# Kernel tuning notes

Measured on AMD Instinct MI355X. Metric: run time of the kernel, lower is better.

Reference implementation:

```python
import jax, jax.numpy as jnp
import numpy as np

N_NODES = 50000
N_EDGES = 800000
D_IN = 256
D_HID = 256
N_CLASSES = 40


def gcn_conv(x, W, b, src, dst, deg_inv_sqrt, n):
    # PyG GCNConv: linear transform first, then normalized scatter-add aggregation.
    x = x @ W                                   # [N, d_out]
    norm = deg_inv_sqrt[src] * deg_inv_sqrt[dst]  # [E+N] sym norm with self-loops
    msgs = x[src] * norm[:, None]               # gather source features
    out = jax.ops.segment_sum(msgs, dst, num_segments=n)
    return out + b


def setup_inputs() -> dict:
    key = jax.random.key(0)
    ks = jax.random.split(key, 6)
    x = jax.random.normal(ks[0], (N_NODES, D_IN), dtype=jnp.float32)
    edge_index = jax.random.randint(ks[1], (2, N_EDGES), 0, N_NODES, dtype=jnp.int64)
    s_in = 1.0 / np.sqrt(D_IN)
    s_h = 1.0 / np.sqrt(D_HID)
    W0 = jax.random.normal(ks[2], (D_IN, D_HID), dtype=jnp.float32) * s_in
    b0 = jnp.zeros((D_HID,), dtype=jnp.float32)
    W1 = jax.random.normal(ks[3], (D_HID, D_HID), dtype=jnp.float32) * s_h
    b1 = jnp.zeros((D_HID,), dtype=jnp.float32)
    W2 = jax.random.normal(ks[4], (D_HID, N_CLASSES), dtype=jnp.float32) * s_h
    b2 = jnp.zeros((N_CLASSES,), dtype=jnp.float32)
    return {"x": x, "edge_index": edge_index, "W0": W0, "b0": b0,
            "W1": W1, "b1": b1, "W2": W2, "b2": b2}


def reference(x, edge_index, W0, b0, W1, b1, W2, b2):
    n = x.shape[0]
    loops = jnp.arange(n, dtype=edge_index.dtype)
    src = jnp.concatenate([edge_index[0], loops])
    dst = jnp.concatenate([edge_index[1], loops])
    # degree (with self-loops) on destination nodes; deg >= 1 so rsqrt is safe
    deg = jax.ops.segment_sum(jnp.ones_like(dst, dtype=x.dtype), dst, num_segments=n)
    deg_inv_sqrt = jax.lax.rsqrt(deg)

    h = gcn_conv(x, W0, b0, src, dst, deg_inv_sqrt, n)
    h = jax.nn.relu(h)  # dropout is identity in eval mode
    h = gcn_conv(h, W1, b1, src, dst, deg_inv_sqrt, n)
    h = jax.nn.relu(h)
    h = gcn_conv(h, W2, b2, src, dst, deg_inv_sqrt, n)
    return jax.nn.log_softmax(h, axis=1)
```

## Files before the change

### kernel.cpp

```cpp
#include <hip/hip_runtime.h>
#include <hip/hip_bf16.h>
#include <cstdint>
#include <cstddef>


typedef unsigned char u8;
typedef unsigned short u16;
typedef unsigned int u32;
typedef __attribute__((ext_vector_type(8))) short bf16x8;
typedef __attribute__((ext_vector_type(4))) float f32x4;
typedef __attribute__((ext_vector_type(2))) float f32x2;

__device__ inline float bfl(u32 u) { return __uint_as_float(u << 16); }
__device__ inline float bfh(u32 u) { return __uint_as_float(u & 0xffff0000u); }
__device__ inline u16 f2bf(float f) {
  __hip_bfloat16 h = __float2bfloat16(f);
  return __builtin_bit_cast(u16, h);
}
__device__ inline u32 pk2bf(float lo, float hi) {
  return ((u32)f2bf(hi) << 16) | (u32)f2bf(lo);
}
__device__ inline u32 pk4fp8(float a, float b, float c, float d) {
  u32 w = __builtin_amdgcn_cvt_pk_fp8_f32(a, b, 0, false);
  w = __builtin_amdgcn_cvt_pk_fp8_f32(c, d, w, true);
  return w;
}
__device__ inline void up4fp8(u32 w, float* a) {
  f32x2 lo = __builtin_amdgcn_cvt_pk_f32_fp8(w, false);
  f32x2 hi = __builtin_amdgcn_cvt_pk_f32_fp8(w, true);
  a[0] += lo[0]; a[1] += lo[1]; a[2] += hi[0]; a[3] += hi[1];
}

__device__ inline void gl_lds16(const u16* g, u16* ldsbase) {
  __builtin_amdgcn_global_load_lds(
      (const __attribute__((address_space(1))) u32*)g,
      (__attribute__((address_space(3))) u32*)ldsbase, 16, 0, 0);
}

__global__ void k_prepcount(const int* __restrict__ dst, int* __restrict__ cnt,
                            int* __restrict__ rank, int E, int CB,
                            const float* __restrict__ W0,
                            const float* __restrict__ W1,
                            const float* __restrict__ W2,
                            u16* __restrict__ Wt0, u16* __restrict__ Wt1,
                            u16* __restrict__ Wt2, int* __restrict__ bflag,
                            u8* __restrict__ zu8, float* __restrict__ z40,
                            int n) {
  if ((int)blockIdx.x < CB) {
    const int e = blockIdx.x * 256 + threadIdx.x;
    if (e < E) rank[e] = atomicAdd(&cnt[dst[e]], 1);
    return;
  }
  const int t = (blockIdx.x - CB) * 256 + threadIdx.x;
  if (t < 65536) {
    const int k = t >> 8, c = t & 255;
    Wt0[c * 256 + k] = f2bf(W0[t]);
    Wt1[c * 256 + k] = f2bf(W1[t]);
  } else if (t < 65536 + 16384) {
    const int t2 = t - 65536;
    const int k = t2 >> 6, nn = t2 & 63;
    const float v = (nn < 40) ? W2[k * 40 + nn] : 0.f;
    Wt2[nn * 256 + k] = f2bf(v);
  }
  const int u = t - (65536 + 16384);
  if (u >= 0) {
    if (u < 64) bflag[u] = 0;
    if (u < 256) zu8[u] = 0;
    if (u < 40) z40[u] = 0.f;
  }
}

__global__ __launch_bounds__(1024) void k_scan(const int* __restrict__ cnt,
                                               int* __restrict__ rs,
                                               float* __restrict__ dis,
                                               int* __restrict__ bval,
                                               int* __restrict__ bpre,
                                               int* __restrict__ bflag, int n) {
  __shared__ int wsum[16];
  __shared__ int sbase;
  const int b = blockIdx.x;
  const int tid = threadIdx.x;
  const int lane = tid & 63, wid = tid >> 6;
  const int i = b * 1024 + tid;
  const int v = (i < n) ? cnt[i] : 0;
  int x = v;
#pragma unroll
  for (int off = 1; off < 64; off <<= 1) {
    int y = __shfl_up(x, off, 64);
    if (lane >= off) x += y;
  }
  if (lane == 63) wsum[wid] = x;
  __syncthreads();
  if (wid == 0) {
    int w = (lane < 16) ? wsum[lane] : 0;
#pragma unroll
    for (int off = 1; off < 16; off <<= 1) {
      int y = __shfl_up(w, off, 64);
      if (lane >= off) w += y;
    }
    if (lane < 16) wsum[lane] = w;
  }
  __syncthreads();
  const int total = wsum[15];
  const int excl = (wid > 0 ? wsum[wid - 1] : 0) + (x - v);

  if (tid == 0) {
    if (b == 0) {
      atomicExch(&bpre[0], total);
      __threadfence();
      atomicExch(&bflag[0], 2);
      sbase = 0;
    } else {
      atomicExch(&bval[b], total);
      __threadfence();
      atomicExch(&bflag[b], 1);
      int run = 0, j = b - 1;
      while (true) {
        int f;
        while ((f = atomicAdd(&bflag[j], 0)) == 0) {}
        if (f == 2) { run += atomicAdd(&bpre[j], 0); break; }
        run += atomicAdd(&bval[j], 0);
        --j;
      }
      atomicExch(&bpre[b], run + total);
      __threadfence();
      atomicExch(&bflag[b], 2);
      sbase = run;
    }
  }
  __syncthreads();
  const int base = sbase;
  if (i < n) {
    rs[i] = base + excl;
    dis[i] = rsqrtf((float)(1 + v));
  }
  if (b == (int)gridDim.x - 1 && tid == 0) rs[n] = base + total;
}

template <bool F32A>
__device__ inline void gemm256_block(const void* __restrict__ Aptr,
                                     const u16* __restrict__ Wt,
                                     const float* __restrict__ dis,
                                     u8* __restrict__ C, int M,
                                     int bx, int by, u16* As, u16* Bs) {
  const int tid = threadIdx.x;
  const int wid = tid >> 6, lane = tid & 63;
  const int wave_m = wid >> 1, wave_n = wid & 1;
  const int m0 = bx * 128, n0 = by * 128;
  const int quad = lane >> 4, col = lane & 15;

  const int srl = lane >> 3;
  const int sseg = lane & 7;

  const int ra = wave_m * 64 + col;
  const int rb = wave_n * 64 + col;

  f32x4 acc[4][4];
#pragma unroll
  for (int i = 0; i < 4; ++i)
#pragma unroll
    for (int j = 0; j < 4; ++j) acc[i][j] = (f32x4){0.f, 0.f, 0.f, 0.f};

  for (int k0 = 0; k0 < 256; k0 += 64) {
#pragma unroll
    for (int blk = 0; blk < 4; ++blk) {
      const int R = wid * 32 + blk * 8;
      const int r = R + srl;
      const int q = (sseg - r) & 7;
      if (F32A) {
        const float* A = (const float*)Aptr;
        const int gm = m0 + r;
        float4 lo = make_float4(0.f, 0.f, 0.f, 0.f), hi = lo;
        if (gm < M) {
          lo = *(const float4*)(A + (size_t)gm * 256 + k0 + q * 8);
          hi = *(const float4*)(A + (size_t)gm * 256 + k0 + q * 8 + 4);
        }
        uint4 w;
        w.x = pk2bf(lo.x, lo.y); w.y = pk2bf(lo.z, lo.w);
        w.z = pk2bf(hi.x, hi.y); w.w = pk2bf(hi.z, hi.w);
        *(uint4*)&As[r * 64 + sseg * 8] = w;
      } else {
        const u16* A = (const u16*)Aptr;
        if (m0 + r < M)
          gl_lds16(A + (size_t)(m0 + r) * 256 + k0 + q * 8, &As[R * 64]);
      }
      gl_lds16(Wt + (size_t)(n0 + r) * 256 + k0 + q * 8, &Bs[R * 64]);
    }
    __syncthreads();

#pragma unroll
    for (int kk = 0; kk < 2; ++kk) {
      bf16x8 af[4], bf[4];
#pragma unroll
      for (int i = 0; i < 4; ++i) {
        const int r = ra + i * 16;
        af[i] = *(const bf16x8*)&As[r * 64 + ((quad + kk * 4 + r) & 7) * 8];
      }
#pragma unroll
      for (int j = 0; j < 4; ++j) {
        const int r = rb + j * 16;
        bf[j] = *(const bf16x8*)&Bs[r * 64 + ((quad + kk * 4 + r) & 7) * 8];
      }
#pragma unroll
      for (int i = 0; i < 4; ++i)
#pragma unroll
        for (int j = 0; j < 4; ++j)
          acc[i][j] = __builtin_amdgcn_mfma_f32_16x16x32_bf16(bf[j], af[i], acc[i][j], 0, 0, 0);
    }
    __syncthreads();
  }

#pragma unroll
  for (int i = 0; i < 4; ++i) {
    const int m = m0 + wave_m * 64 + i * 16 + col;
    if (m < M) {
      const float dd = dis[m];
#pragma unroll
      for (int j = 0; j < 4; ++j) {
        const int n = n0 + wave_n * 64 + j * 16 + quad * 4;
        const u32 w = pk4fp8(acc[i][j][0] * dd, acc[i][j][1] * dd,
                             acc[i][j][2] * dd, acc[i][j][3] * dd);
        *(u32*)(C + (size_t)m * 256 + n) = w;
      }
    }
  }
}

__global__ __launch_bounds__(256) void k_gemmfill(
    const float* __restrict__ x, const u16* __restrict__ Wt0,
    const float* __restrict__ dis, u8* __restrict__ C, int M,
    const int* __restrict__ src, const int* __restrict__ dst,
    const int* __restrict__ rank, const int* __restrict__ rs,
    int* __restrict__ csr, int E, int FB) {
  __shared__ u16 As[128 * 64];
  __shared__ u16 Bs[128 * 64];
  if ((int)blockIdx.x < FB) {
    const int e = blockIdx.x * 256 + threadIdx.x;
    if (e < E) csr[rs[dst[e]] + rank[e]] = src[e];
    return;
  }
  const int bb = blockIdx.x - FB;
  gemm256_block<true>(x, Wt0, dis, C, M, bb >> 1, bb & 1, As, Bs);
}

__global__ __launch_bounds__(256) void k_gemm256(const u16* __restrict__ A,
                                                 const u16* __restrict__ Wt,
                                                 const float* __restrict__ dis,
                                                 u8* __restrict__ C, int M) {
  __shared__ u16 As[128 * 64];
  __shared__ u16 Bs[128 * 64];
  gemm256_block<false>(A, Wt, dis, C, M, blockIdx.x, blockIdx.y, As, Bs);
}

__global__ __launch_bounds__(256) void k_agg256(const u8* __restrict__ u,
                                                const int* __restrict__ rs,
                                                const int* __restrict__ csr,
                                                const float* __restrict__ dis,
                                                const float* __restrict__ b,
                                                u16* __restrict__ out, int n,
                                                int d0, int d1) {
  const int wid = threadIdx.x >> 6, lane = threadIdx.x & 63;
  const int d = d0 + blockIdx.x * 4 + wid;
  if (d >= d1) return;
  const int q = lane >> 4, sl = lane & 15;
  const int cb = sl * 16;
  float a[16] = {0.f, 0.f, 0.f, 0.f, 0.f, 0.f, 0.f, 0.f,
                 0.f, 0.f, 0.f, 0.f, 0.f, 0.f, 0.f, 0.f};
  {
    const int sidx = q ? n : d;
    const uint4 v = *(const uint4*)(u + (size_t)sidx * 256 + cb);
    up4fp8(v.x, a); up4fp8(v.y, a + 4); up4fp8(v.z, a + 8); up4fp8(v.w, a + 12);
  }
  const int p1 = rs[d + 1];
  for (int p = rs[d]; p < p1; p += 16) {
    int idx[4];
#pragma unroll
    for (int i = 0; i < 4; ++i) {
      const int e = p + 4 * i + q;
      idx[i] = (e < p1) ? csr[e] : n;
    }
    uint4 v[4];
#pragma unroll
    for (int i = 0; i < 4; ++i)
      v[i] = *(const uint4*)(u + (size_t)idx[i] * 256 + cb);
#pragma unroll
    for (int i = 0; i < 4; ++i) {
      up4fp8(v[i].x, a); up4fp8(v[i].y, a + 4);
      up4fp8(v[i].z, a + 8); up4fp8(v[i].w, a + 12);
    }
  }
#pragma unroll
  for (int j = 0; j < 16; ++j) {
    a[j] += __shfl_xor(a[j], 16, 64);
    a[j] += __shfl_xor(a[j], 32, 64);
  }
  if (q == 0) {
    const float dd = dis[d];
    uint4 o0, o1;
    const float4 b0 = *(const float4*)(b + cb);
    const float4 b1 = *(const float4*)(b + cb + 4);
    const float4 b2 = *(const float4*)(b + cb + 8);
    const float4 b3 = *(const float4*)(b + cb + 12);
    o0.x = pk2bf(fmaxf(dd * a[0] + b0.x, 0.f), fmaxf(dd * a[1] + b0.y, 0.f));
    o0.y = pk2bf(fmaxf(dd * a[2] + b0.z, 0.f), fmaxf(dd * a[3] + b0.w, 0.f));
    o0.z = pk2bf(fmaxf(dd * a[4] + b1.x, 0.f), fmaxf(dd * a[5] + b1.y, 0.f));
    o0.w = pk2bf(fmaxf(dd * a[6] + b1.z, 0.f), fmaxf(dd * a[7] + b1.w, 0.f));
    o1.x = pk2bf(fmaxf(dd * a[8] + b2.x, 0.f), fmaxf(dd * a[9] + b2.y, 0.f));
    o1.y = pk2bf(fmaxf(dd * a[10] + b2.z, 0.f), fmaxf(dd * a[11] + b2.w, 0.f));
    o1.z = pk2bf(fmaxf(dd * a[12] + b3.x, 0.f), fmaxf(dd * a[13] + b3.y, 0.f));
    o1.w = pk2bf(fmaxf(dd * a[14] + b3.z, 0.f), fmaxf(dd * a[15] + b3.w, 0.f));
    *(uint4*)(out + (size_t)d * 256 + cb) = o0;
    *(uint4*)(out + (size_t)d * 256 + cb + 8) = o1;
  }
}

__global__ __launch_bounds__(256) void k_gemm40(const u16* __restrict__ A,
                                                const u16* __restrict__ Wt2,
                                                const float* __restrict__ dis,
                                                float* __restrict__ C, int M) {
  const int wv = threadIdx.x >> 6, lane = threadIdx.x & 63;
  const int quad = lane >> 4, col = lane & 15;
  const int m0 = blockIdx.x * 128 + wv * 32;
  f32x4 acc[2][3];
#pragma unroll
  for (int i = 0; i < 2; ++i)
#pragma unroll
    for (int j = 0; j < 3; ++j) acc[i][j] = (f32x4){0.f, 0.f, 0.f, 0.f};
  for (int k0 = 0; k0 < 256; k0 += 32) {
    bf16x8 af[2], bf[3];
#pragma unroll
    for (int i = 0; i < 2; ++i) {
      int row = m0 + i * 16 + col;
      row = (row < M) ? row : (M - 1);
      af[i] = *(const bf16x8*)(A + (size_t)row * 256 + k0 + quad * 8);
    }
#pragma unroll
    for (int j = 0; j < 3; ++j)
      bf[j] = *(const bf16x8*)(Wt2 + (size_t)(j * 16 + col) * 256 + k0 + quad * 8);
#pragma unroll
    for (int i = 0; i < 2; ++i)
#pragma unroll
      for (int j = 0; j < 3; ++j)
        acc[i][j] = __builtin_amdgcn_mfma_f32_16x16x32_bf16(bf[j], af[i], acc[i][j], 0, 0, 0);
  }
#pragma unroll
  for (int i = 0; i < 2; ++i) {
    const int m = m0 + i * 16 + col;
    if (m < M) {
      const float dd = dis[m];
#pragma unroll
      for (int j = 0; j < 3; ++j) {
        const int nn = j * 16 + quad * 4;
        if (nn < 40) {
          float4 o = make_float4(acc[i][j][0] * dd, acc[i][j][1] * dd,
                                 acc[i][j][2] * dd, acc[i][j][3] * dd);
          *(float4*)(C + (size_t)m * 40 + nn) = o;
        }
      }
    }
  }
}

__global__ __launch_bounds__(256) void k_agg40(const float* __restrict__ u,
                                               const int* __restrict__ rs,
                                               const int* __restrict__ csr,
                                               const float* __restrict__ dis,
                                               const float* __restrict__ b,
                                               float* __restrict__ out, int n) {
  const int wid = threadIdx.x >> 6, lane = threadIdx.x & 63;
  const int d = blockIdx.x * 4 + wid;
  if (d >= n) return;
  const int slot = lane / 20;
  const int sl = lane % 20;
  const bool act = slot < 3;
  const int col = sl * 2;
  float a0 = 0.f, a1 = 0.f;
  if (slot == 0) {
    const float2 v = *(const float2*)(u + (size_t)d * 40 + col);
    a0 = v.x; a1 = v.y;
  }
  const int p1 = rs[d + 1];
  for (int p = rs[d]; p < p1; p += 12) {
    int idx[4];
#pragma unroll
    for (int i = 0; i < 4; ++i) {
      const int e = p + 3 * i + slot;
      idx[i] = (act && e < p1) ? csr[e] : n;
    }
    float2 v[4];
#pragma unroll
    for (int i = 0; i < 4; ++i)
      v[i] = *(const float2*)(u + (size_t)idx[i] * 40 + col);
#pragma unroll
    for (int i = 0; i < 4; ++i) { a0 += v[i].x; a1 += v[i].y; }
  }
  a0 += __shfl(a0, lane + 20, 64) + __shfl(a0, lane + 40, 64);
  a1 += __shfl(a1, lane + 20, 64) + __shfl(a1, lane + 40, 64);
  float l0 = -INFINITY, l1 = -INFINITY;
  if (lane < 20) {
    const float dd = dis[d];
    l0 = dd * a0 + b[col];
    l1 = dd * a1 + b[col + 1];
  }
  float mx = fmaxf(l0, l1);
#pragma unroll
  for (int off = 16; off; off >>= 1) mx = fmaxf(mx, __shfl_xor(mx, off, 32));
  float e0 = (lane < 20) ? expf(l0 - mx) : 0.f;
  float e1 = (lane < 20) ? expf(l1 - mx) : 0.f;
  float sm = e0 + e1;
#pragma unroll
  for (int off = 16; off; off >>= 1) sm += __shfl_xor(sm, off, 32);
  if (lane < 20) {
    const float ls = mx + logf(sm);
    float2 o = make_float2(l0 - ls, l1 - ls);
    *(float2*)(out + (size_t)d * 40 + col) = o;
  }
}

extern "C" void kernel_launch(void* const* d_in, const int* in_sizes, int n_in,
                              void* d_out, int out_size, void* d_ws, size_t ws_size,
                              hipStream_t stream) {
  const float* x  = (const float*)d_in[0];
  const int*   ei = (const int*)d_in[1];
  const float* W0 = (const float*)d_in[2];
  const float* b0 = (const float*)d_in[3];
  const float* W1 = (const float*)d_in[4];
  const float* b1 = (const float*)d_in[5];
  const float* W2 = (const float*)d_in[6];
  const float* b2 = (const float*)d_in[7];
  float* out = (float*)d_out;

  const int N = in_sizes[0] / 256;
  const int E = in_sizes[1] / 2;
  const int* src = ei;
  const int* dst = ei + E;

  char* p = (char*)d_ws;
  auto carve = [&](size_t bytes) {
    char* q = p;
    p += (bytes + 255) & ~(size_t)255;
    return q;
  };
  u8*    uf8   = (u8*)carve((size_t)(N + 1) * 256);
  u16*   h     = (u16*)carve((size_t)N * 256 * 2);
  float* u40   = (float*)carve((size_t)(N + 1) * 40 * 4);
  u16*   Wt0   = (u16*)carve(256 * 256 * 2);
  u16*   Wt1   = (u16*)carve(256 * 256 * 2);
  u16*   Wt2   = (u16*)carve(64 * 256 * 2);
  float* dis   = (float*)carve((size_t)N * 4);
  int*   cnt   = (int*)carve((size_t)N * 4);
  int*   rs    = (int*)carve((size_t)(N + 1) * 4);
  int*   rank  = (int*)carve((size_t)E * 4);
  int*   csr   = (int*)carve((size_t)(E + 16) * 4);
  int*   bval  = (int*)carve(64 * 4);
  int*   bpre  = (int*)carve(64 * 4);
  int*   bflag = (int*)carve(64 * 4);

  const int CB = (E + 255) / 256;
  const int prep_items = 65536 + 16384 + 256;
  const int PB = (prep_items + 255) / 256;
  const int nb = (N + 1023) / 1024;
  const int GB = ((N + 127) / 128) * 2;

  hipMemsetAsync(cnt, 0, (size_t)N * 4, stream);

  k_prepcount<<<CB + PB, 256, 0, stream>>>(dst, cnt, rank, E, CB,
                                           W0, W1, W2, Wt0, Wt1, Wt2, bflag,
                                           uf8 + (size_t)N * 256,
                                           u40 + (size_t)N * 40, N);
  k_scan<<<nb, 1024, 0, stream>>>(cnt, rs, dis, bval, bpre, bflag, N);
  k_gemmfill<<<CB + GB, 256, 0, stream>>>(x, Wt0, dis, uf8, N,
                                          src, dst, rank, rs, csr, E, CB);

  const int Nh = N / 2;
  const int ga1 = (Nh + 3) / 4, ga2 = (N - Nh + 3) / 4;

  k_agg256<<<ga1, 256, 0, stream>>>(uf8, rs, csr, dis, b0, h, N, 0, Nh);
  k_agg256<<<ga2, 256, 0, stream>>>(uf8, rs, csr, dis, b0, h, N, Nh, N);
  k_gemm256<<<dim3((N + 127) / 128, 2), 256, 0, stream>>>(h, Wt1, dis, uf8, N);
  k_agg256<<<ga1, 256, 0, stream>>>(uf8, rs, csr, dis, b1, h, N, 0, Nh);
  k_agg256<<<ga2, 256, 0, stream>>>(uf8, rs, csr, dis, b1, h, N, Nh, N);
  k_gemm40<<<(N + 127) / 128, 256, 0, stream>>>(h, Wt2, dis, u40, N);
  k_agg40<<<(N + 3) / 4, 256, 0, stream>>>(u40, rs, csr, dis, b2, out, N);
}
```

Measured before the change: 334.8 us.

## Pre-convert x to bf16, store layer-3 messages in fp8, merge split aggregations

Converts x to bf16 in the prep kernel so the first GEMM can use direct global-to-LDS loads instead of converting fp32 in-loop. Stores the 40-class projected features as fp8 instead of fp32, and reworks the final aggregation to handle 6 edges per pass with 4 fp8 values per lane. It also replaces the two half-range aggregation launches per layer with one full launch and reorders block roles in the fused kernels. This adds an extra 25MB bf16 round trip for x and more fp8 quantization error in the last layer.

```diff
diff --git a/kernel.cpp b/kernel.cpp
--- a/kernel.cpp
+++ b/kernel.cpp
@@ -11,8 +11,6 @@
 typedef __attribute__((ext_vector_type(4))) float f32x4;
 typedef __attribute__((ext_vector_type(2))) float f32x2;
 
-__device__ inline float bfl(u32 u) { return __uint_as_float(u << 16); }
-__device__ inline float bfh(u32 u) { return __uint_as_float(u & 0xffff0000u); }
 __device__ inline u16 f2bf(float f) {
   __hip_bfloat16 h = __float2bfloat16(f);
   return __builtin_bit_cast(u16, h);
@@ -37,37 +35,51 @@
       (__attribute__((address_space(3))) u32*)ldsbase, 16, 0, 0);
 }
 
-__global__ void k_prepcount(const int* __restrict__ dst, int* __restrict__ cnt,
-                            int* __restrict__ rank, int E, int CB,
-                            const float* __restrict__ W0,
-                            const float* __restrict__ W1,
-                            const float* __restrict__ W2,
-                            u16* __restrict__ Wt0, u16* __restrict__ Wt1,
-                            u16* __restrict__ Wt2, int* __restrict__ bflag,
-                            u8* __restrict__ zu8, float* __restrict__ z40,
-                            int n) {
-  if ((int)blockIdx.x < CB) {
-    const int e = blockIdx.x * 256 + threadIdx.x;
-    if (e < E) rank[e] = atomicAdd(&cnt[dst[e]], 1);
+__global__ void k_prepcvtcount(const float* __restrict__ W0,
+                               const float* __restrict__ W1,
+                               const float* __restrict__ W2,
+                               u16* __restrict__ Wt0, u16* __restrict__ Wt1,
+                               u16* __restrict__ Wt2, int* __restrict__ bflag,
+                               u8* __restrict__ zu8, u8* __restrict__ z40,
+                               const float* __restrict__ x, u16* __restrict__ xb,
+                               int total8,
+                               const int* __restrict__ dst, int* __restrict__ cnt,
+                               int* __restrict__ rank, int E,
+                               int PB, int VB, int n) {
+  const int bid = blockIdx.x;
+  if (bid < PB) {
+    const int t = bid * 256 + threadIdx.x;
+    if (t < 65536) {
+      const int k = t >> 8, c = t & 255;
+      Wt0[c * 256 + k] = f2bf(W0[t]);
+      Wt1[c * 256 + k] = f2bf(W1[t]);
+    } else if (t < 65536 + 16384) {
+      const int t2 = t - 65536;
+      const int k = t2 >> 6, nn = t2 & 63;
+      const float v = (nn < 40) ? W2[k * 40 + nn] : 0.f;
+      Wt2[nn * 256 + k] = f2bf(v);
+    } else {
+      const int u = t - (65536 + 16384);
+      if (u < 64) bflag[u] = 0;
+      if (u < 256) zu8[u] = 0;
+      if (u < 40) z40[u] = 0;
+    }
     return;
   }
-  const int t = (blockIdx.x - CB) * 256 + threadIdx.x;
-  if (t < 65536) {
-    const int k = t >> 8, c = t & 255;
-    Wt0[c * 256 + k] = f2bf(W0[t]);
-    Wt1[c * 256 + k] = f2bf(W1[t]);
-  } else if (t < 65536 + 16384) {
-    const int t2 = t - 65536;
-    const int k = t2 >> 6, nn = t2 & 63;
-    const float v = (nn < 40) ? W2[k * 40 + nn] : 0.f;
-    Wt2[nn * 256 + k] = f2bf(v);
-  }
-  const int u = t - (65536 + 16384);
-  if (u >= 0) {
-    if (u < 64) bflag[u] = 0;
-    if (u < 256) zu8[u] = 0;
-    if (u < 40) z40[u] = 0.f;
-  }
+  if (bid < PB + VB) {
+    const int i = (bid - PB) * 256 + threadIdx.x;
+    if (i < total8) {
+      const float4 lo = ((const float4*)x)[2 * i];
+      const float4 hi = ((const float4*)x)[2 * i + 1];
+      uint4 w;
+      w.x = pk2bf(lo.x, lo.y); w.y = pk2bf(lo.z, lo.w);
+      w.z = pk2bf(hi.x, hi.y); w.w = pk2bf(hi.z, hi.w);
+      ((uint4*)xb)[i] = w;
+    }
+    return;
+  }
+  const int e = (bid - PB - VB) * 256 + threadIdx.x;
+  if (e < E) rank[e] = atomicAdd(&cnt[dst[e]], 1);
 }
 
 __global__ __launch_bounds__(1024) void k_scan(const int* __restrict__ cnt,
@@ -137,12 +149,11 @@
   if (b == (int)gridDim.x - 1 && tid == 0) rs[n] = base + total;
 }
 
-template <bool F32A>
-__device__ inline void gemm256_block(const void* __restrict__ Aptr,
-                                     const u16* __restrict__ Wt,
-                                     const float* __restrict__ dis,
-                                     u8* __restrict__ C, int M,
-                                     int bx, int by, u16* As, u16* Bs) {
+__device__ inline void gemm256_body(const u16* __restrict__ A,
+                                    const u16* __restrict__ Wt,
+                                    const float* __restrict__ dis,
+                                    u8* __restrict__ C, int M,
+                                    int bx, int by, u16* As, u16* Bs) {
   const int tid = threadIdx.x;
   const int wid = tid >> 6, lane = tid & 63;
   const int wave_m = wid >> 1, wave_n = wid & 1;
@@ -167,23 +178,8 @@
       const int R = wid * 32 + blk * 8;
       const int r = R + srl;
       const int q = (sseg - r) & 7;
-      if (F32A) {
-        const float* A = (const float*)Aptr;
-        const int gm = m0 + r;
-        float4 lo = make_float4(0.f, 0.f, 0.f, 0.f), hi = lo;
-        if (gm < M) {
-          lo = *(const float4*)(A + (size_t)gm * 256 + k0 + q * 8);
-          hi = *(const float4*)(A + (size_t)gm * 256 + k0 + q * 8 + 4);
-        }
-        uint4 w;
-        w.x = pk2bf(lo.x, lo.y); w.y = pk2bf(lo.z, lo.w);
-        w.z = pk2bf(hi.x, hi.y); w.w = pk2bf(hi.z, hi.w);
-        *(uint4*)&As[r * 64 + sseg * 8] = w;
-      } else {
-        const u16* A = (const u16*)Aptr;
-        if (m0 + r < M)
-          gl_lds16(A + (size_t)(m0 + r) * 256 + k0 + q * 8, &As[R * 64]);
-      }
+      if (m0 + r < M)
+        gl_lds16(A + (size_t)(m0 + r) * 256 + k0 + q * 8, &As[R * 64]);
       gl_lds16(Wt + (size_t)(n0 + r) * 256 + k0 + q * 8, &Bs[R * 64]);
     }
     __syncthreads();
@@ -227,20 +223,19 @@
 }
 
 __global__ __launch_bounds__(256) void k_gemmfill(
-    const float* __restrict__ x, const u16* __restrict__ Wt0,
+    const u16* __restrict__ xb, const u16* __restrict__ Wt0,
     const float* __restrict__ dis, u8* __restrict__ C, int M,
     const int* __restrict__ src, const int* __restrict__ dst,
     const int* __restrict__ rank, const int* __restrict__ rs,
-    int* __restrict__ csr, int E, int FB) {
+    int* __restrict__ csr, int E, int GB) {
   __shared__ u16 As[128 * 64];
   __shared__ u16 Bs[128 * 64];
-  if ((int)blockIdx.x < FB) {
-    const int e = blockIdx.x * 256 + threadIdx.x;
+  if ((int)blockIdx.x >= GB) {
+    const int e = (blockIdx.x - GB) * 256 + threadIdx.x;
     if (e < E) csr[rs[dst[e]] + rank[e]] = src[e];
     return;
   }
-  const int bb = blockIdx.x - FB;
-  gemm256_block<true>(x, Wt0, dis, C, M, bb >> 1, bb & 1, As, Bs);
+  gemm256_body(xb, Wt0, dis, C, M, blockIdx.x >> 1, blockIdx.x & 1, As, Bs);
 }
 
 __global__ __launch_bounds__(256) void k_gemm256(const u16* __restrict__ A,
@@ -249,7 +244,7 @@
                                                  u8* __restrict__ C, int M) {
   __shared__ u16 As[128 * 64];
   __shared__ u16 Bs[128 * 64];
-  gemm256_block<false>(A, Wt, dis, C, M, blockIdx.x, blockIdx.y, As, Bs);
+  gemm256_body(A, Wt, dis, C, M, blockIdx.x, blockIdx.y, As, Bs);
 }
 
 __global__ __launch_bounds__(256) void k_agg256(const u8* __restrict__ u,
@@ -257,11 +252,10 @@
                                                 const int* __restrict__ csr,
                                                 const float* __restrict__ dis,
                                                 const float* __restrict__ b,
-                                                u16* __restrict__ out, int n,
-                                                int d0, int d1) {
+                                                u16* __restrict__ out, int n) {
   const int wid = threadIdx.x >> 6, lane = threadIdx.x & 63;
-  const int d = d0 + blockIdx.x * 4 + wid;
-  if (d >= d1) return;
+  const int d = blockIdx.x * 4 + wid;
+  if (d >= n) return;
   const int q = lane >> 4, sl = lane & 15;
   const int cb = sl * 16;
   float a[16] = {0.f, 0.f, 0.f, 0.f, 0.f, 0.f, 0.f, 0.f,
@@ -317,7 +311,7 @@
 __global__ __launch_bounds__(256) void k_gemm40(const u16* __restrict__ A,
                                                 const u16* __restrict__ Wt2,
                                                 const float* __restrict__ dis,
-                                                float* __restrict__ C, int M) {
+                                                u8* __restrict__ C, int M) {
   const int wv = threadIdx.x >> 6, lane = threadIdx.x & 63;
   const int quad = lane >> 4, col = lane & 15;
   const int m0 = blockIdx.x * 128 + wv * 32;
@@ -352,16 +346,16 @@
       for (int j = 0; j < 3; ++j) {
         const int nn = j * 16 + quad * 4;
         if (nn < 40) {
-          float4 o = make_float4(acc[i][j][0] * dd, acc[i][j][1] * dd,
-                                 acc[i][j][2] * dd, acc[i][j][3] * dd);
-          *(float4*)(C + (size_t)m * 40 + nn) = o;
+          const u32 w = pk4fp8(acc[i][j][0] * dd, acc[i][j][1] * dd,
+                               acc[i][j][2] * dd, acc[i][j][3] * dd);
+          *(u32*)(C + (size_t)m * 40 + nn) = w;
         }
       }
     }
   }
 }
 
-__global__ __launch_bounds__(256) void k_agg40(const float* __restrict__ u,
+__global__ __launch_bounds__(256) void k_agg40(const u8* __restrict__ u,
                                                const int* __restrict__ rs,
                                                const int* __restrict__ csr,
                                                const float* __restrict__ dis,
@@ -370,50 +364,64 @@
   const int wid = threadIdx.x >> 6, lane = threadIdx.x & 63;
   const int d = blockIdx.x * 4 + wid;
   if (d >= n) return;
-  const int slot = lane / 20;
-  const int sl = lane % 20;
-  const bool act = slot < 3;
-  const int col = sl * 2;
-  float a0 = 0.f, a1 = 0.f;
+  const int slot = lane / 10;
+  const int sl = lane % 10;
+  const bool act = slot < 6;
+  float a[4] = {0.f, 0.f, 0.f, 0.f};
   if (slot == 0) {
-    const float2 v = *(const float2*)(u + (size_t)d * 40 + col);
-    a0 = v.x; a1 = v.y;
+    const u32 v = *(const u32*)(u + (size_t)d * 40 + sl * 4);
+    up4fp8(v, a);
   }
   const int p1 = rs[d + 1];
-  for (int p = rs[d]; p < p1; p += 12) {
+  for (int p = rs[d]; p < p1; p += 24) {
     int idx[4];
 #pragma unroll
     for (int i = 0; i < 4; ++i) {
-      const int e = p + 3 * i + slot;
+      const int e = p + 6 * i + slot;
       idx[i] = (act && e < p1) ? csr[e] : n;
     }
-    float2 v[4];
+    u32 v[4];
 #pragma unroll
     for (int i = 0; i < 4; ++i)
-      v[i] = *(const float2*)(u + (size_t)idx[i] * 40 + col);
-#pragma unroll
-    for (int i = 0; i < 4; ++i) { a0 += v[i].x; a1 += v[i].y; }
-  }
-  a0 += __shfl(a0, lane + 20, 64) + __shfl(a0, lane + 40, 64);
-  a1 += __shfl(a1, lane + 20, 64) + __shfl(a1, lane + 40, 64);
-  float l0 = -INFINITY, l1 = -INFINITY;
-  if (lane < 20) {
+      v[i] = *(const u32*)(u + (size_t)idx[i] * 40 + sl * 4);
+#pragma unroll
+    for (int i = 0; i < 4; ++i) up4fp8(v[i], a);
+  }
+#pragma unroll
+  for (int k = 0; k < 4; ++k) {
+    const float t = __shfl(a[k], lane + 30, 64);
+    a[k] += t;
+  }
+#pragma unroll
+  for (int k = 0; k < 4; ++k) {
+    const float t1 = __shfl(a[k], lane + 10, 64);
+    const float t2 = __shfl(a[k], lane + 20, 64);
+    a[k] += t1 + t2;
+  }
+  float l[4];
+  float mx = -INFINITY;
+  const bool head = lane < 10;
+  if (head) {
     const float dd = dis[d];
-    l0 = dd * a0 + b[col];
-    l1 = dd * a1 + b[col + 1];
-  }
-  float mx = fmaxf(l0, l1);
-#pragma unroll
-  for (int off = 16; off; off >>= 1) mx = fmaxf(mx, __shfl_xor(mx, off, 32));
-  float e0 = (lane < 20) ? expf(l0 - mx) : 0.f;
-  float e1 = (lane < 20) ? expf(l1 - mx) : 0.f;
-  float sm = e0 + e1;
-#pragma unroll
-  for (int off = 16; off; off >>= 1) sm += __shfl_xor(sm, off, 32);
-  if (lane < 20) {
+#pragma unroll
+    for (int k = 0; k < 4; ++k) {
+      l[k] = dd * a[k] + b[lane * 4 + k];
+      mx = fmaxf(mx, l[k]);
+    }
+  }
+#pragma unroll
+  for (int off = 8; off; off >>= 1) mx = fmaxf(mx, __shfl_xor(mx, off, 64));
+  float sm = 0.f;
+  if (head) {
+#pragma unroll
+    for (int k = 0; k < 4; ++k) sm += expf(l[k] - mx);
+  }
+#pragma unroll
+  for (int off = 8; off; off >>= 1) sm += __shfl_xor(sm, off, 64);
+  if (head) {
     const float ls = mx + logf(sm);
-    float2 o = make_float2(l0 - ls, l1 - ls);
-    *(float2*)(out + (size_t)d * 40 + col) = o;
+    float4 o = make_float4(l[0] - ls, l[1] - ls, l[2] - ls, l[3] - ls);
+    *(float4*)(out + (size_t)d * 40 + lane * 4) = o;
   }
 }
 
@@ -441,9 +449,10 @@
     p += (bytes + 255) & ~(size_t)255;
     return q;
   };
+  u16*   xb    = (u16*)carve((size_t)N * 256 * 2);
   u8*    uf8   = (u8*)carve((size_t)(N + 1) * 256);
   u16*   h     = (u16*)carve((size_t)N * 256 * 2);
-  float* u40   = (float*)carve((size_t)(N + 1) * 40 * 4);
+  u8*    u40   = (u8*)carve((size_t)(N + 1) * 40);
   u16*   Wt0   = (u16*)carve(256 * 256 * 2);
   u16*   Wt1   = (u16*)carve(256 * 256 * 2);
   u16*   Wt2   = (u16*)carve(64 * 256 * 2);
@@ -451,35 +460,31 @@
   int*   cnt   = (int*)carve((size_t)N * 4);
   int*   rs    = (int*)carve((size_t)(N + 1) * 4);
   int*   rank  = (int*)carve((size_t)E * 4);
-  int*   csr   = (int*)carve((size_t)(E + 16) * 4);
+  int*   csr   = (int*)carve((size_t)(E + 32) * 4);
   int*   bval  = (int*)carve(64 * 4);
   int*   bpre  = (int*)carve(64 * 4);
   int*   bflag = (int*)carve(64 * 4);
 
+  const int PB = (65536 + 16384 + 256 + 255) / 256;
+  const int total8 = N * 256 / 8;
+  const int VB = (total8 + 255) / 256;
   const int CB = (E + 255) / 256;
-  const int prep_items = 65536 + 16384 + 256;
-  const int PB = (prep_items + 255) / 256;
+  const int GB = ((N + 127) / 128) * 2;
   const int nb = (N + 1023) / 1024;
-  const int GB = ((N + 127) / 128) * 2;
+  const int agrid = (N + 3) / 4;
 
   hipMemsetAsync(cnt, 0, (size_t)N * 4, stream);
 
-  k_prepcount<<<CB + PB, 256, 0, stream>>>(dst, cnt, rank, E, CB,
-                                           W0, W1, W2, Wt0, Wt1, Wt2, bflag,
-                                           uf8 + (size_t)N * 256,
-                                           u40 + (size_t)N * 40, N);
+  k_prepcvtcount<<<PB + VB + CB, 256, 0, stream>>>(
+      W0, W1, W2, Wt0, Wt1, Wt2, bflag,
+      uf8 + (size_t)N * 256, u40 + (size_t)N * 40,
+      x, xb, total8, dst, cnt, rank, E, PB, VB, N);
   k_scan<<<nb, 1024, 0, stream>>>(cnt, rs, dis, bval, bpre, bflag, N);
-  k_gemmfill<<<CB + GB, 256, 0, stream>>>(x, Wt0, dis, uf8, N,
-                                          src, dst, rank, rs, csr, E, CB);
-
-  const int Nh = N / 2;
-  const int ga1 = (Nh + 3) / 4, ga2 = (N - Nh + 3) / 4;
-
-  k_agg256<<<ga1, 256, 0, stream>>>(uf8, rs, csr, dis, b0, h, N, 0, Nh);
-  k_agg256<<<ga2, 256, 0, stream>>>(uf8, rs, csr, dis, b0, h, N, Nh, N);
+  k_gemmfill<<<GB + CB, 256, 0, stream>>>(xb, Wt0, dis, uf8, N,
+                                          src, dst, rank, rs, csr, E, GB);
+  k_agg256<<<agrid, 256, 0, stream>>>(uf8, rs, csr, dis, b0, h, N);
   k_gemm256<<<dim3((N + 127) / 128, 2), 256, 0, stream>>>(h, Wt1, dis, uf8, N);
-  k_agg256<<<ga1, 256, 0, stream>>>(uf8, rs, csr, dis, b1, h, N, 0, Nh);
-  k_agg256<<<ga2, 256, 0, stream>>>(uf8, rs, csr, dis, b1, h, N, Nh, N);
+  k_agg256<<<agrid, 256, 0, stream>>>(uf8, rs, csr, dis, b1, h, N);
   k_gemm40<<<(N + 127) / 128, 256, 0, stream>>>(h, Wt2, dis, u40, N);
-  k_agg40<<<(N + 3) / 4, 256, 0, stream>>>(u40, rs, csr, dis, b2, out, N);
-}
+  k_agg40<<<agrid, 256, 0, stream>>>(u40, rs, csr, dis, b2, out, N);
+}
```

Measured after the change: 306.3 us. 1.09x faster.
